# Kernel tuning notes

Hardware: AMD Instinct MI355X
Metric: run time of the kernel (lower is better)

## Reference

```python
import jax, jax.numpy as jnp
import numpy as np

N = 100000   # nodes
E = 1600000  # edges
C = 128      # num_features == out_channels
L = 3        # num_layers


def setup_inputs() -> dict:
    key = jax.random.key(0)
    ks = jax.random.split(key, 7)
    x = jax.random.normal(ks[0], (N, C), dtype=jnp.float32)
    edge_index = jax.random.randint(ks[1], (2, E), 0, N, dtype=jnp.int64)
    # GatedGraphConv per-layer linear weights [L, C, C]
    weight = jax.random.normal(ks[2], (L, C, C), dtype=jnp.float32) / np.sqrt(C)
    # shared GRUCell params (torch layout: [3C, C] rows = r, z, n)
    w_ih = jax.random.normal(ks[3], (3 * C, C), dtype=jnp.float32) / np.sqrt(C)
    w_hh = jax.random.normal(ks[4], (3 * C, C), dtype=jnp.float32) / np.sqrt(C)
    b_ih = jax.random.normal(ks[5], (3 * C,), dtype=jnp.float32) * 0.01
    b_hh = jax.random.normal(ks[6], (3 * C,), dtype=jnp.float32) * 0.01
    return {"x": x, "edge_index": edge_index, "weight": weight,
            "w_ih": w_ih, "w_hh": w_hh, "b_ih": b_ih, "b_hh": b_hh}


def _gru_cell(inp, h, w_ih, w_hh, b_ih, b_hh):
    gi = inp @ w_ih.T + b_ih  # [N, 3C]
    gh = h @ w_hh.T + b_hh    # [N, 3C]
    i_r, i_z, i_n = jnp.split(gi, 3, axis=1)
    h_r, h_z, h_n = jnp.split(gh, 3, axis=1)
    r = jax.nn.sigmoid(i_r + h_r)
    z = jax.nn.sigmoid(i_z + h_z)
    n = jnp.tanh(i_n + r * h_n)
    return (1.0 - z) * n + z * h


def reference(x, edge_index, weight, w_ih, w_hh, b_ih, b_hh):
    src, dst = edge_index[0], edge_index[1]
    n_nodes = x.shape[0]
    # mean aggregation denominators (in-degree, 0-degree nodes -> 0 output)
    counts = jax.ops.segment_sum(jnp.ones(src.shape[0], dtype=x.dtype), dst,
                                 num_segments=n_nodes)
    denom = jnp.maximum(counts, 1.0)[:, None]
    h = x
    for i in range(weight.shape[0]):
        m = h @ weight[i]                                   # [N, C]
        agg = jax.ops.segment_sum(m[src], dst, num_segments=n_nodes) / denom
        h = _gru_cell(agg, h, w_ih, w_hh, b_ih, b_hh)
    # x.mean(1).unsqueeze(1) -> [N, 1], then tanh
    return jnp.tanh(jnp.mean(h, axis=1, keepdims=True))
```

## Files before the change

kernel.cpp:

```cpp
#include <hip/hip_runtime.h>
#include <math.h>

#define NN 100000
#define NE 1600000
#define CC 128
#define C3 384
#define SCAN_B 256
#define SCAN_NB ((NN + SCAN_B - 1) / SCAN_B)

typedef __attribute__((ext_vector_type(4))) float f4;
typedef __attribute__((ext_vector_type(8))) short s8;

__device__ __forceinline__ float sigmoidf_(float x) { return 1.0f / (1.0f + __expf(-x)); }
__device__ __forceinline__ float tanhf_(float x) { return 2.0f / (1.0f + __expf(-2.0f * x)) - 1.0f; }

__device__ __forceinline__ short f2bf(float x) {
    unsigned u = __float_as_uint(x);
    unsigned r = (u + 0x7fffu + ((u >> 16) & 1u)) >> 16;
    return (short)r;
}
__device__ __forceinline__ float bf2f(short s) {
    return __uint_as_float(((unsigned)(unsigned short)s) << 16);
}

__device__ __forceinline__ int detect_flag(const int* e32) {
    int allz = 1;
#pragma unroll
    for (int i = 0; i < 32; i++)
        if (e32[2 * i + 1] != 0) allz = 0;
    return allz;
}

__device__ __forceinline__ int edge_val(const void* edges, int f, long long idx) {
    return f ? (int)((const long long*)edges)[idx] : ((const int*)edges)[idx];
}

__global__ void k_count(const void* __restrict__ edges, int* __restrict__ counts) {
    __shared__ int sf;
    if (threadIdx.x == 0) sf = detect_flag((const int*)edges);
    __syncthreads();
    int f = sf;
    int e = blockIdx.x * blockDim.x + threadIdx.x;
    if (e < NE) {
        int d = edge_val(edges, f, (long long)NE + e);
        atomicAdd(&counts[d], 1);
    }
}

__global__ void k_scan1(const int* __restrict__ counts, int* __restrict__ bsum) {
    __shared__ int red[4];
    int t = threadIdx.x;
    int i = blockIdx.x * SCAN_B + t;
    int v = (i < NN) ? counts[i] : 0;
#pragma unroll
    for (int off = 32; off; off >>= 1) v += __shfl_down(v, off);
    if ((t & 63) == 0) red[t >> 6] = v;
    __syncthreads();
    if (t == 0) bsum[blockIdx.x] = red[0] + red[1] + red[2] + red[3];
}

__global__ void k_scan2(const int* __restrict__ bsum, int* __restrict__ boff,
                        int* __restrict__ coarse_cursor) {
    __shared__ int lds[512];
    int t = threadIdx.x;
    int v = (t < SCAN_NB) ? bsum[t] : 0;
    lds[t] = v;
    __syncthreads();
    for (int off = 1; off < 512; off <<= 1) {
        int u = (t >= off) ? lds[t - off] : 0;
        __syncthreads();
        lds[t] += u;
        __syncthreads();
    }
    if (t < SCAN_NB) {
        int ex = lds[t] - v;
        boff[t] = ex;
        coarse_cursor[t] = ex;
    }
}

__global__ void k_scan3(const int* __restrict__ counts, const int* __restrict__ boff,
                        int* __restrict__ rowptr, float* __restrict__ inv_denom) {
    __shared__ int lds[SCAN_B];
    int t = threadIdx.x;
    int i = blockIdx.x * SCAN_B + t;
    int v = (i < NN) ? counts[i] : 0;
    lds[t] = v;
    __syncthreads();
    for (int off = 1; off < SCAN_B; off <<= 1) {
        int u = (t >= off) ? lds[t - off] : 0;
        __syncthreads();
        lds[t] += u;
        __syncthreads();
    }
    if (i < NN) {
        rowptr[i] = boff[blockIdx.x] + lds[t] - v;
        inv_denom[i] = 1.0f / (float)((v > 1) ? v : 1);
    }
    if (i == 0) rowptr[NN] = NE;
}

__global__ __launch_bounds__(1024) void k_part(const void* __restrict__ edges,
                                               int* __restrict__ coarse_cursor,
                                               uint2* __restrict__ tmp) {
    __shared__ int hist[SCAN_NB];
    __shared__ int base[SCAN_NB];
    __shared__ int sf;
    int t = threadIdx.x;
    if (t == 0) sf = detect_flag((const int*)edges);
    long long e0 = (long long)blockIdx.x * 8192;

    for (int c = t; c < SCAN_NB; c += 1024) hist[c] = 0;
    __syncthreads();
    int f = sf;

    int src[8], dst[8];
#pragma unroll
    for (int i = 0; i < 8; i++) {
        long long e = e0 + i * 1024 + t;
        if (e < NE) {
            src[i] = edge_val(edges, f, e);
            dst[i] = edge_val(edges, f, NE + e);
            atomicAdd(&hist[dst[i] >> 8], 1);
        } else {
            dst[i] = -1;
        }
    }
    __syncthreads();
    for (int c = t; c < SCAN_NB; c += 1024) {
        int h = hist[c];
        base[c] = (h > 0) ? atomicAdd(&coarse_cursor[c], h) : 0;
        hist[c] = 0;
    }
    __syncthreads();
#pragma unroll
    for (int i = 0; i < 8; i++) {
        if (dst[i] >= 0) {
            int c = dst[i] >> 8;
            int off = atomicAdd(&hist[c], 1);
            tmp[base[c] + off] = make_uint2((unsigned)src[i], (unsigned)dst[i]);
        }
    }
}

__global__ void k_fine(const uint2* __restrict__ tmp, const int* __restrict__ rowptr,
                       int* __restrict__ csr_src) {
    __shared__ int cur[256];
    int c = blockIdx.x;
    int t = threadIdx.x;
    int d = c * 256 + t;
    cur[t] = (d <= NN) ? rowptr[d < NN ? d : NN] : NE;
    __syncthreads();
    int start = rowptr[c * 256];
    int endd = (c * 256 + 256 <= NN) ? rowptr[c * 256 + 256] : NE;
    for (int p = start + t; p < endd; p += 256) {
        uint2 pr = tmp[p];
        int slot = atomicAdd(&cur[pr.y & 255], 1);
        csr_src[slot] = (int)pr.x;
    }
}

__global__ void k_prep(const float* __restrict__ weight, const float* __restrict__ w_ih,
                       const float* __restrict__ w_hh, const float* __restrict__ b_ih,
                       const float* __restrict__ b_hh,
                       short* __restrict__ B1hi, short* __restrict__ B2hi,
                       float* __restrict__ bvec) {
    const int P1 = 3 * C3 * CC;
    int gid = blockIdx.x * blockDim.x + threadIdx.x;
    if (gid < P1) {
        int i = gid / (C3 * CC);
        int rem = gid % (C3 * CC);
        int j = rem / CC;
        int k = rem % CC;
        const float* Wr = weight + i * CC * CC + k * CC;
        const float* ir = w_ih + j * CC;
        float v = 0.f;
#pragma unroll 4
        for (int c = 0; c < CC; c++) v += Wr[c] * ir[c];
        short hi = f2bf(v);
        if (j < 256) B1hi[i * 65536 + j * 256 + k] = hi;
        else B2hi[i * 32768 + (j - 256) * 128 + k] = hi;
    } else if (gid < 2 * P1) {
        int g = gid - P1;
        int i = g / (C3 * CC);
        int rem = g % (C3 * CC);
        int j = rem / CC;
        int k = rem % CC;
        short hi = f2bf(w_hh[j * CC + k]);
        if (j < 256) B1hi[i * 65536 + j * 256 + 128 + k] = hi;
        else B2hi[i * 32768 + (j - 256 + 128) * 128 + k] = hi;
    } else if (gid < 2 * P1 + 512) {
        int j = gid - 2 * P1;
        float v;
        if (j < 256) v = b_ih[j] + b_hh[j];
        else if (j < 384) v = b_ih[j];
        else v = b_hh[j - 128];
        bvec[j] = v;
    }
}

__global__ void k_cvt(const float* __restrict__ x, unsigned short* __restrict__ hhi,
                      unsigned short* __restrict__ hlo) {
    long long g = ((long long)blockIdx.x * 256 + threadIdx.x) * 8;
    float4 v0 = *(const float4*)(x + g);
    float4 v1 = *(const float4*)(x + g + 4);
    float f[8] = {v0.x, v0.y, v0.z, v0.w, v1.x, v1.y, v1.z, v1.w};
    s8 oh, ol;
#pragma unroll
    for (int q = 0; q < 8; q++) {
        short hi = f2bf(f[q]);
        oh[q] = hi;
        ol[q] = f2bf(f[q] - bf2f(hi));
    }
    *(s8*)(hhi + g) = oh;
    *(s8*)(hlo + g) = ol;
}

__global__ __launch_bounds__(512, 4) void k_fused(
    const unsigned short* __restrict__ hhi_i, const unsigned short* __restrict__ hlo_i,
    unsigned short* __restrict__ hhi_o, unsigned short* __restrict__ hlo_o,
    const int* __restrict__ rowptr, const int* __restrict__ csr_src,
    const float* __restrict__ inv_denom,
    const short* __restrict__ B1hi, const short* __restrict__ B2hi,
    const float* __restrict__ bvec, float* __restrict__ out) {
    __shared__ short Ahi[16384];
    __shared__ short Alo[16384];
    __shared__ float osum[64];
    int t = threadIdx.x;
    long long nb = (long long)blockIdx.x * 64;
    int wv = t >> 6;
    int L = t & 63;

    if (out && t < 64) osum[t] = 0.f;

#pragma unroll
    for (int i = 0; i < 2; i++) {
        int ci = t + 512 * i;
        int rr = ci >> 4;
        int c = ci & 15;
        int c4 = 16 + c;
        long long row = nb + rr;
        if (row >= NN) row = NN - 1;
        int off = (c4 >> 2) * 2048 + (rr >> 4) * 512 + (rr & 15) * 32 + (c4 & 3) * 8;
        long long gsrc = row * CC + c * 8;
        *(s8*)&Ahi[off] = *(const s8*)(hhi_i + gsrc);
        *(s8*)&Alo[off] = *(const s8*)(hlo_i + gsrc);
    }

    {
        int q = L >> 4;
        int l16 = L & 15;
#pragma unroll
        for (int pass = 0; pass < 2; pass++) {
            int rr = wv * 8 + pass * 4 + q;
            long long rowc = nb + rr;
            if (rowc >= NN) rowc = NN - 1;
            int lo = rowptr[rowc], hi = rowptr[rowc + 1];
            float acc0[8] = {0, 0, 0, 0, 0, 0, 0, 0};
            float acc1[8] = {0, 0, 0, 0, 0, 0, 0, 0};
            int e = lo;
            for (; e + 3 < hi; e += 4) {
                int s0 = csr_src[e];
                int s1 = csr_src[e + 1];
                int s2 = csr_src[e + 2];
                int s3 = csr_src[e + 3];
                s8 v0 = ((const s8*)(hhi_i + (long long)s0 * CC))[l16];
                s8 v1 = ((const s8*)(hhi_i + (long long)s1 * CC))[l16];
                s8 v2 = ((const s8*)(hhi_i + (long long)s2 * CC))[l16];
                s8 v3 = ((const s8*)(hhi_i + (long long)s3 * CC))[l16];
#pragma unroll
                for (int k = 0; k < 8; k++) {
                    acc0[k] += bf2f(v0[k]) + bf2f(v2[k]);
                    acc1[k] += bf2f(v1[k]) + bf2f(v3[k]);
                }
            }
            for (; e + 1 < hi; e += 2) {
                int s0 = csr_src[e];
                int s1 = csr_src[e + 1];
                s8 v0 = ((const s8*)(hhi_i + (long long)s0 * CC))[l16];
                s8 v1 = ((const s8*)(hhi_i + (long long)s1 * CC))[l16];
#pragma unroll
                for (int k = 0; k < 8; k++) {
                    acc0[k] += bf2f(v0[k]);
                    acc1[k] += bf2f(v1[k]);
                }
            }
            if (e < hi) {
                int s0 = csr_src[e];
                s8 v0 = ((const s8*)(hhi_i + (long long)s0 * CC))[l16];
#pragma unroll
                for (int k = 0; k < 8; k++) acc0[k] += bf2f(v0[k]);
            }
            float inv = inv_denom[rowc];
            s8 vh, vl;
#pragma unroll
            for (int k = 0; k < 8; k++) {
                float f = (acc0[k] + acc1[k]) * inv;
                short hi16 = f2bf(f);
                vh[k] = hi16;
                vl[k] = f2bf(f - bf2f(hi16));
            }
            int off = (l16 >> 2) * 2048 + (rr >> 4) * 512 + (rr & 15) * 32 + (l16 & 3) * 8;
            *(s8*)&Ahi[off] = vh;
            *(s8*)&Alo[off] = vl;
        }
    }
    __syncthreads();

    int lm = L & 15;
    int lq = L >> 4;
    int j = wv * 16 + lm;

    f4 aR[4], aZ[4], aN[4], aH[4];
    {
        float bR = bvec[j], bZ = bvec[128 + j], bN = bvec[256 + j], bH = bvec[384 + j];
#pragma unroll
        for (int ch = 0; ch < 4; ch++) {
            aR[ch] = (f4){bR, bR, bR, bR};
            aZ[ch] = (f4){bZ, bZ, bZ, bZ};
            aN[ch] = (f4){bN, bN, bN, bN};
            aH[ch] = (f4){bH, bH, bH, bH};
        }
    }

#pragma unroll
    for (int ks = 0; ks < 8; ks++) {
        int o1 = ks * 32 + lq * 8;
        s8 bRh = *(const s8*)(B1hi + j * 256 + o1);
        s8 bZh = *(const s8*)(B1hi + (128 + j) * 256 + o1);
        int rowG = (ks < 4) ? j : (128 + j);
        int o2 = (ks & 3) * 32 + lq * 8;
        s8 bGh = *(const s8*)(B2hi + rowG * 128 + o2);
#pragma unroll
        for (int ch = 0; ch < 4; ch++) {
            int aoff = ks * 2048 + ch * 512 + lm * 32 + lq * 8;
            s8 ah = *(const s8*)&Ahi[aoff];
            s8 al = *(const s8*)&Alo[aoff];
            aR[ch] = __builtin_amdgcn_mfma_f32_16x16x32_bf16(ah, bRh, aR[ch], 0, 0, 0);
            aR[ch] = __builtin_amdgcn_mfma_f32_16x16x32_bf16(al, bRh, aR[ch], 0, 0, 0);
            aZ[ch] = __builtin_amdgcn_mfma_f32_16x16x32_bf16(ah, bZh, aZ[ch], 0, 0, 0);
            aZ[ch] = __builtin_amdgcn_mfma_f32_16x16x32_bf16(al, bZh, aZ[ch], 0, 0, 0);
            if (ks < 4) {
                aN[ch] = __builtin_amdgcn_mfma_f32_16x16x32_bf16(ah, bGh, aN[ch], 0, 0, 0);
                aN[ch] = __builtin_amdgcn_mfma_f32_16x16x32_bf16(al, bGh, aN[ch], 0, 0, 0);
            } else {
                aH[ch] = __builtin_amdgcn_mfma_f32_16x16x32_bf16(ah, bGh, aH[ch], 0, 0, 0);
                aH[ch] = __builtin_amdgcn_mfma_f32_16x16x32_bf16(al, bGh, aH[ch], 0, 0, 0);
            }
        }
    }

    {
        int c4 = 16 + (j >> 3);
        int obase = (c4 >> 2) * 2048 + (c4 & 3) * 8 + (j & 7);
#pragma unroll
        for (int ch = 0; ch < 4; ch++) {
#pragma unroll
            for (int r = 0; r < 4; r++) {
                int node = ch * 16 + lq * 4 + r;
                int off = obase + ch * 512 + (node & 15) * 32;
                float hp = bf2f(Ahi[off]) + bf2f(Alo[off]);
                float rg = sigmoidf_(aR[ch][r]);
                float zg = sigmoidf_(aZ[ch][r]);
                float nv = tanhf_(aN[ch][r] + rg * aH[ch][r]);
                float val = (1.f - zg) * nv + zg * hp;
                long long gnode = nb + node;
                if (out) {
                    atomicAdd(&osum[node], val);
                } else if (gnode < NN) {
                    long long gd = gnode * CC + j;
                    short vh = f2bf(val);
                    hhi_o[gd] = (unsigned short)vh;
                    hlo_o[gd] = (unsigned short)f2bf(val - bf2f(vh));
                }
            }
        }
    }
    if (out) {
        __syncthreads();
        if (t < 64 && nb + t < NN)
            out[nb + t] = tanhf_(osum[t] * (1.0f / 128.0f));
    }
}

extern "C" void kernel_launch(void* const* d_in, const int* in_sizes, int n_in,
                              void* d_out, int out_size, void* d_ws, size_t ws_size,
                              hipStream_t stream) {
    const float* x = (const float*)d_in[0];
    const void* edges = d_in[1];
    const float* weight = (const float*)d_in[2];
    const float* w_ih = (const float*)d_in[3];
    const float* w_hh = (const float*)d_in[4];
    const float* b_ih = (const float*)d_in[5];
    const float* b_hh = (const float*)d_in[6];
    float* out = (float*)d_out;

    char* ws = (char*)d_ws;
    size_t off = 0;
    auto alloc = [&](size_t bytes) -> char* {
        char* p = ws + off;
        off += (bytes + 255) & ~(size_t)255;
        return p;
    };
    int* counts = (int*)alloc((size_t)NN * 4);
    int* rowptr = (int*)alloc((size_t)(NN + 1) * 4);
    int* csr_src = (int*)alloc((size_t)NE * 4);
    float* inv_den = (float*)alloc((size_t)NN * 4);
    int* bsum = (int*)alloc((size_t)SCAN_NB * 4);
    int* boff = (int*)alloc((size_t)SCAN_NB * 4);
    int* coarse_cursor = (int*)alloc((size_t)SCAN_NB * 4);
    uint2* tmp = (uint2*)alloc((size_t)NE * 8);
    short* B1hi = (short*)alloc((size_t)3 * 65536 * 2);
    short* B2hi = (short*)alloc((size_t)3 * 32768 * 2);
    float* bvec = (float*)alloc(512 * 4);
    unsigned short* hhi0 = (unsigned short*)alloc((size_t)NN * CC * 2);
    unsigned short* hlo0 = (unsigned short*)alloc((size_t)NN * CC * 2);
    unsigned short* hhi1 = (unsigned short*)alloc((size_t)NN * CC * 2);
    unsigned short* hlo1 = (unsigned short*)alloc((size_t)NN * CC * 2);

    hipMemsetAsync(counts, 0, (size_t)NN * 4, stream);

    k_count<<<(NE + 255) / 256, 256, 0, stream>>>(edges, counts);
    k_scan1<<<SCAN_NB, SCAN_B, 0, stream>>>(counts, bsum);
    k_scan2<<<1, 512, 0, stream>>>(bsum, boff, coarse_cursor);
    k_scan3<<<SCAN_NB, SCAN_B, 0, stream>>>(counts, boff, rowptr, inv_den);
    k_part<<<(NE + 8191) / 8192, 1024, 0, stream>>>(edges, coarse_cursor, tmp);
    k_fine<<<SCAN_NB, 256, 0, stream>>>(tmp, rowptr, csr_src);
    int prep_threads = 2 * 3 * C3 * CC + 512;
    k_prep<<<(prep_threads + 255) / 256, 256, 0, stream>>>(weight, w_ih, w_hh, b_ih, b_hh,
                                                           B1hi, B2hi, bvec);
    k_cvt<<<(NN * CC) / 2048, 256, 0, stream>>>(x, hhi0, hlo0);

    const int blocks = (NN + 63) / 64;
    unsigned short* hi_in = hhi0;  unsigned short* lo_in = hlo0;
    unsigned short* hi_out = hhi1; unsigned short* lo_out = hlo1;
    for (int i = 0; i < 3; i++) {
        float* outp = (i == 2) ? out : nullptr;
        k_fused<<<blocks, 512, 0, stream>>>(hi_in, lo_in, hi_out, lo_out,
                                            rowptr, csr_src, inv_den,
                                            B1hi + (size_t)i * 65536,
                                            B2hi + (size_t)i * 32768,
                                            bvec, outp);
        unsigned short* th = hi_in; hi_in = hi_out; hi_out = th;
        unsigned short* tl = lo_in; lo_in = lo_out; lo_out = tl;
    }
}
```

Baseline: 641.7 us.

## Balance edge gather across block threads with LDS atomic accumulation

Replaces the per-row neighbor aggregation, where each quarter-wave handles one destination row, with an edge-balanced split. Each 16-lane group takes an equal slice of the block's edge range, finds its starting row by binary search over a shared rowptr copy, and flushes partial sums into an fp32 LDS buffer with atomicAdd at row boundaries. This removes load imbalance from skewed in-degrees within a block. In exchange it adds LDS zeroing, extra barriers, LDS atomics and a second conversion pass that reuses the A tile memory.

```diff
diff --git a/kernel.cpp b/kernel.cpp
--- a/kernel.cpp
+++ b/kernel.cpp
@@ -223,15 +223,31 @@
     const float* __restrict__ inv_denom,
     const short* __restrict__ B1hi, const short* __restrict__ B2hi,
     const float* __restrict__ bvec, float* __restrict__ out) {
-    __shared__ short Ahi[16384];
-    __shared__ short Alo[16384];
+    __shared__ short AA[32768];
     __shared__ float osum[64];
+    __shared__ int rp[65];
+    short* Ahi = AA;
+    short* Alo = AA + 16384;
     int t = threadIdx.x;
     long long nb = (long long)blockIdx.x * 64;
     int wv = t >> 6;
     int L = t & 63;
 
     if (out && t < 64) osum[t] = 0.f;
+    if (t < 65) {
+        long long ridx = nb + t;
+        rp[t] = rowptr[ridx > NN ? NN : ridx];
+    }
+
+    {
+        float* a0 = (float*)AA;
+        float* a1 = (float*)(AA + 16384);
+#pragma unroll
+        for (int i = 0; i < 8; i++) {
+            a0[t + 512 * i] = 0.f;
+            a1[t + 512 * i] = 0.f;
+        }
+    }
 
 #pragma unroll
     for (int i = 0; i < 2; i++) {
@@ -246,20 +262,42 @@
         *(s8*)&Ahi[off] = *(const s8*)(hhi_i + gsrc);
         *(s8*)&Alo[off] = *(const s8*)(hlo_i + gsrc);
     }
+    __syncthreads();
 
     {
-        int q = L >> 4;
-        int l16 = L & 15;
-#pragma unroll
-        for (int pass = 0; pass < 2; pass++) {
-            int rr = wv * 8 + pass * 4 + q;
-            long long rowc = nb + rr;
-            if (rowc >= NN) rowc = NN - 1;
-            int lo = rowptr[rowc], hi = rowptr[rowc + 1];
-            float acc0[8] = {0, 0, 0, 0, 0, 0, 0, 0};
-            float acc1[8] = {0, 0, 0, 0, 0, 0, 0, 0};
-            int e = lo;
-            for (; e + 3 < hi; e += 4) {
+        int qw = t >> 4;
+        int l16 = t & 15;
+        int ebeg = rp[0], eend = rp[64];
+        int tot = eend - ebeg;
+        int per = (tot + 31) >> 5;
+        int e0 = ebeg + qw * per;
+        int e1 = e0 + per;
+        if (e1 > eend) e1 = eend;
+        if (e0 < eend) {
+            int lo2 = 0, hi2 = 64;
+            while (hi2 - lo2 > 1) {
+                int mid = (lo2 + hi2) >> 1;
+                if (e0 >= rp[mid]) lo2 = mid;
+                else hi2 = mid;
+            }
+            int cur = lo2;
+            float acc[8] = {0, 0, 0, 0, 0, 0, 0, 0};
+            auto aggrow = [&](int r) -> float* {
+                return (float*)(AA + ((r >> 5) << 14)) + (r & 31) * 128 + l16 * 8;
+            };
+            auto adv = [&](int ei) {
+                if (ei >= rp[cur + 1]) {
+                    float* ap = aggrow(cur);
+#pragma unroll
+                    for (int k = 0; k < 8; k++) {
+                        atomicAdd(&ap[k], acc[k]);
+                        acc[k] = 0.f;
+                    }
+                    do { cur++; } while (ei >= rp[cur + 1]);
+                }
+            };
+            int e = e0;
+            for (; e + 3 < e1; e += 4) {
                 int s0 = csr_src[e];
                 int s1 = csr_src[e + 1];
                 int s2 = csr_src[e + 2];
@@ -268,42 +306,64 @@
                 s8 v1 = ((const s8*)(hhi_i + (long long)s1 * CC))[l16];
                 s8 v2 = ((const s8*)(hhi_i + (long long)s2 * CC))[l16];
                 s8 v3 = ((const s8*)(hhi_i + (long long)s3 * CC))[l16];
-#pragma unroll
-                for (int k = 0; k < 8; k++) {
-                    acc0[k] += bf2f(v0[k]) + bf2f(v2[k]);
-                    acc1[k] += bf2f(v1[k]) + bf2f(v3[k]);
-                }
-            }
-            for (; e + 1 < hi; e += 2) {
-                int s0 = csr_src[e];
-                int s1 = csr_src[e + 1];
-                s8 v0 = ((const s8*)(hhi_i + (long long)s0 * CC))[l16];
-                s8 v1 = ((const s8*)(hhi_i + (long long)s1 * CC))[l16];
-#pragma unroll
-                for (int k = 0; k < 8; k++) {
-                    acc0[k] += bf2f(v0[k]);
-                    acc1[k] += bf2f(v1[k]);
-                }
-            }
-            if (e < hi) {
+                adv(e);
+#pragma unroll
+                for (int k = 0; k < 8; k++) acc[k] += bf2f(v0[k]);
+                adv(e + 1);
+#pragma unroll
+                for (int k = 0; k < 8; k++) acc[k] += bf2f(v1[k]);
+                adv(e + 2);
+#pragma unroll
+                for (int k = 0; k < 8; k++) acc[k] += bf2f(v2[k]);
+                adv(e + 3);
+#pragma unroll
+                for (int k = 0; k < 8; k++) acc[k] += bf2f(v3[k]);
+            }
+            for (; e < e1; e++) {
                 int s0 = csr_src[e];
                 s8 v0 = ((const s8*)(hhi_i + (long long)s0 * CC))[l16];
-#pragma unroll
-                for (int k = 0; k < 8; k++) acc0[k] += bf2f(v0[k]);
-            }
+                adv(e);
+#pragma unroll
+                for (int k = 0; k < 8; k++) acc[k] += bf2f(v0[k]);
+            }
+            {
+                float* ap = aggrow(cur);
+#pragma unroll
+                for (int k = 0; k < 8; k++) atomicAdd(&ap[k], acc[k]);
+            }
+        }
+    }
+    __syncthreads();
+
+    {
+        int l16 = t & 15;
+        int q = L >> 4;
+        s8 vh0, vl0, vh1, vl1;
+        int off0, off1;
+#pragma unroll
+        for (int pass = 0; pass < 2; pass++) {
+            int rr = wv * 8 + pass * 4 + q;
+            long long rowc = nb + rr;
+            if (rowc >= NN) rowc = NN - 1;
             float inv = inv_denom[rowc];
+            const float* ap = (const float*)(AA + ((rr >> 5) << 14)) + (rr & 31) * 128 + l16 * 8;
             s8 vh, vl;
 #pragma unroll
             for (int k = 0; k < 8; k++) {
-                float f = (acc0[k] + acc1[k]) * inv;
+                float f = ap[k] * inv;
                 short hi16 = f2bf(f);
                 vh[k] = hi16;
                 vl[k] = f2bf(f - bf2f(hi16));
             }
             int off = (l16 >> 2) * 2048 + (rr >> 4) * 512 + (rr & 15) * 32 + (l16 & 3) * 8;
-            *(s8*)&Ahi[off] = vh;
-            *(s8*)&Alo[off] = vl;
-        }
+            if (pass == 0) { vh0 = vh; vl0 = vl; off0 = off; }
+            else { vh1 = vh; vl1 = vl; off1 = off; }
+        }
+        __syncthreads();
+        *(s8*)&Ahi[off0] = vh0;
+        *(s8*)&Alo[off0] = vl0;
+        *(s8*)&Ahi[off1] = vh1;
+        *(s8*)&Alo[off1] = vl1;
     }
     __syncthreads();
 
```

After: 813.8 us. 26.8% more time.
